# Kernel tuning notes

Measured on AMD Instinct MI355X. Metric: run time of the kernel, lower is better.

## Reference

```python
import jax, jax.numpy as jnp
import numpy as np

D_MODEL = 1024
NUM_HEADS = 16
HEAD_DIM = D_MODEL // NUM_HEADS


def setup_inputs() -> dict:
    key = jax.random.key(0)
    ks = jax.random.split(key, 9)
    B, S, D = 4, 2048, D_MODEL
    scale = 1.0 / np.sqrt(D)
    x = jax.random.normal(ks[0], (B, S, D), dtype=jnp.float32)
    wq = jax.random.normal(ks[1], (D, D), dtype=jnp.float32) * scale
    wk = jax.random.normal(ks[2], (D, D), dtype=jnp.float32) * scale
    wv = jax.random.normal(ks[3], (D, D), dtype=jnp.float32) * scale
    wo = jax.random.normal(ks[4], (D, D), dtype=jnp.float32) * scale
    bq = jax.random.normal(ks[5], (D,), dtype=jnp.float32) * 0.02
    bk = jax.random.normal(ks[6], (D,), dtype=jnp.float32) * 0.02
    bv = jax.random.normal(ks[7], (D,), dtype=jnp.float32) * 0.02
    bo = jax.random.normal(ks[8], (D,), dtype=jnp.float32) * 0.02
    return {"x": x, "wq": wq, "bq": bq, "wk": wk, "bk": bk,
            "wv": wv, "bv": bv, "wo": wo, "bo": bo}


def _split_heads(t):  # [B,S,D] -> [B,H,S,Dh]
    B, S, _ = t.shape
    return t.reshape(B, S, NUM_HEADS, HEAD_DIM).transpose(0, 2, 1, 3)


def reference(x, wq, bq, wk, bk, wv, bv, wo, bo):
    B, S, D = x.shape
    q = _split_heads(x @ wq + bq)  # [B,H,S,Dh]
    k = _split_heads(x @ wk + bk)
    v = _split_heads(x @ wv + bv)
    scores = jnp.einsum("bhqd,bhkd->bhqk", q, k) / jnp.sqrt(
        jnp.asarray(HEAD_DIM, dtype=x.dtype))
    causal = jnp.tril(jnp.ones((S, S), dtype=bool))  # [S,S]
    scores = jnp.where(causal, scores, jnp.finfo(scores.dtype).min)
    attn = jax.nn.softmax(scores, axis=-1)
    ctx = jnp.einsum("bhqk,bhkd->bhqd", attn, v)  # [B,H,S,Dh]
    ctx = ctx.transpose(0, 2, 1, 3).reshape(B, S, D)
    return ctx @ wo + bo
```

## Files before the change

kernel.cpp:

```cpp
#include <hip/hip_runtime.h>
#include <hip/hip_bf16.h>
#include <stdint.h>

#define DMODEL 1024
#define NH 16
#define DH 64
#define BATCH 4
#define SEQ 2048

#if __has_builtin(__builtin_amdgcn_exp2f)
#define EXP2F(x) __builtin_amdgcn_exp2f(x)
#else
#define EXP2F(x) exp2f(x)
#endif

typedef __attribute__((ext_vector_type(8))) short short8;
typedef __attribute__((ext_vector_type(4))) float f32x4;
typedef __attribute__((ext_vector_type(4))) ushort ushort4v;

__device__ __forceinline__ ushort f2bf(float f) {
    union { float f; unsigned u; } v; v.f = f;
    unsigned r = v.u + 0x7fffu + ((v.u >> 16) & 1u);
    return (ushort)(r >> 16);
}

__global__ __launch_bounds__(256) void prep_inputs(
    const float* __restrict__ x, ushort* __restrict__ xbf,
    const float* __restrict__ s0, const float* __restrict__ s1,
    const float* __restrict__ s2, const float* __restrict__ s3,
    ushort* __restrict__ d0, ushort* __restrict__ d1,
    ushort* __restrict__ d2, ushort* __restrict__ d3) {
    __shared__ ushort tile[64][65];
    const int bid = blockIdx.x;
    if (bid < 4096) {
        const size_t i = ((size_t)bid * 256 + threadIdx.x) * 8;
        float4 a = *(const float4*)(x + i);
        float4 b = *(const float4*)(x + i + 4);
        short8 r;
        r[0] = (short)f2bf(a.x); r[1] = (short)f2bf(a.y);
        r[2] = (short)f2bf(a.z); r[3] = (short)f2bf(a.w);
        r[4] = (short)f2bf(b.x); r[5] = (short)f2bf(b.y);
        r[6] = (short)f2bf(b.z); r[7] = (short)f2bf(b.w);
        *(short8*)(xbf + i) = r;
        return;
    }
    const int r = bid - 4096;
    const int z = r >> 8;
    const float* src = (z == 0) ? s0 : (z == 1) ? s1 : (z == 2) ? s2 : s3;
    ushort* dst = (z == 0) ? d0 : (z == 1) ? d1 : (z == 2) ? d2 : d3;
    const int bx = (r & 15) * 64;
    const int by = ((r >> 4) & 15) * 64;
    const int tx = threadIdx.x & 63, ty = threadIdx.x >> 6;
    #pragma unroll
    for (int i = 0; i < 64; i += 4)
        tile[ty + i][tx] = f2bf(src[(size_t)(by + ty + i) * DMODEL + bx + tx]);
    __syncthreads();
    #pragma unroll
    for (int i = 0; i < 64; i += 4)
        dst[(size_t)(bx + ty + i) * DMODEL + by + tx] = tile[tx][ty + i];
}

#define BK 32
#define NT 32

template <int MODE>
__global__ __launch_bounds__(256, 3) void gemm_tile(
    const ushort* __restrict__ A, const ushort* __restrict__ Bt,
    const float* __restrict__ b0, const float* __restrict__ b1,
    const float* __restrict__ b2,
    void* __restrict__ o0v, void* __restrict__ o1v, void* __restrict__ o2v) {
    __shared__ __align__(16) ushort lds[24576];
    const int tid  = threadIdx.x;
    const int lane = tid & 63;
    const int wv   = tid >> 6;

    const int bid = blockIdx.x;
    const int by  = ((bid & 7) << 3) | ((bid >> 3) & 7);
    const int bx  = bid >> 6;
    const int mBase = by * 128, nBase = bx * 128;

    const int wm = (wv >> 1) * 64;
    const int wn = (wv & 1) * 64;
    const int frow = lane & 15;
    const int fq   = lane >> 4;
    const int cA   = ((((fq ^ (frow >> 1)) & 3) << 1) | (frow & 1)) << 3;
    const int roff = (frow >> 1) * 64 + cA;

    const int sr   = tid >> 3;
    const int c8   = tid & 7;
    const int grow = (sr << 1) | (c8 & 1);
    const int gkc8 = (((c8 >> 1) ^ sr) & 3) * 8;
    const ushort* gA = A  + (size_t)(mBase + grow) * DMODEL + gkc8;
    const ushort* gB = Bt + (size_t)(nBase + grow) * DMODEL + gkc8;
    const int ldsw = wv * 512;

    f32x4 acc[4][4];
    #pragma unroll
    for (int i = 0; i < 4; ++i)
        #pragma unroll
        for (int j = 0; j < 4; ++j) acc[i][j] = (f32x4){0.f, 0.f, 0.f, 0.f};

#define STG(gp, off) __builtin_amdgcn_global_load_lds( \
    (const __attribute__((address_space(1))) void*)(gp), \
    (__attribute__((address_space(3))) void*)&lds[(off) + ldsw], 16, 0, 0)
#define STAGE_A(sb, u, h) STG(gA + (size_t)(h) * 64 * DMODEL + (u) * BK, \
                              (sb) + (h) * 2048)
#define STAGE_B(sb, u, h) STG(gB + (size_t)(h) * 64 * DMODEL + (u) * BK, \
                              (sb) + 4096 + (h) * 2048)

    STAGE_A(0, 0, 0); STAGE_A(0, 0, 1); STAGE_B(0, 0, 0); STAGE_B(0, 0, 1);
    STAGE_A(8192, 1, 0); STAGE_A(8192, 1, 1);
    STAGE_B(8192, 1, 0); STAGE_B(8192, 1, 1);
    asm volatile("s_waitcnt vmcnt(4)" ::: "memory");
    __builtin_amdgcn_s_barrier();

    int sc = 0;
    #pragma unroll 1
    for (int u = 0; u < NT; ++u) {
        const int scB = sc * 8192;
        const int sp  = (sc == 0) ? 2 : sc - 1;
        const int spB = sp * 8192;
        const ushort* bufA = &lds[scB + wm * 32];
        const ushort* bufB = &lds[scB + 4096 + wn * 32];

        if (u + 2 < NT) {
            STAGE_A(spB, u + 2, 0); STAGE_A(spB, u + 2, 1);
            STAGE_B(spB, u + 2, 0); STAGE_B(spB, u + 2, 1);
        }

        short8 af[4], bf[4];
        #pragma unroll
        for (int f = 0; f < 4; ++f)
            af[f] = *(const short8*)&bufA[f * 512 + roff];
        #pragma unroll
        for (int j = 0; j < 4; ++j)
            bf[j] = *(const short8*)&bufB[j * 512 + roff];
        __builtin_amdgcn_s_setprio(1);
        #pragma unroll
        for (int f = 0; f < 4; ++f)
            #pragma unroll
            for (int j = 0; j < 4; ++j)
                acc[f][j] = __builtin_amdgcn_mfma_f32_16x16x32_bf16(
                    af[f], bf[j], acc[f][j], 0, 0, 0);
        __builtin_amdgcn_s_setprio(0);

        if (u + 2 < NT)       { asm volatile("s_waitcnt vmcnt(4)" ::: "memory"); }
        else if (u + 2 == NT) { asm volatile("s_waitcnt vmcnt(0)" ::: "memory"); }
        __builtin_amdgcn_s_barrier();
        sc = (sc == 2) ? 0 : sc + 1;
    }
#undef STG
#undef STAGE_A
#undef STAGE_B

    const int orow = fq * 4;
    const int ocol = frow;

    if (MODE == 1) {
        #pragma unroll
        for (int i = 0; i < 4; ++i)
            #pragma unroll
            for (int j = 0; j < 4; ++j)
                #pragma unroll
                for (int r = 0; r < 4; ++r) {
                    const int m = mBase + wm + i * 16 + orow + r;
                    const int n = nBase + wn + j * 16 + ocol;
                    ((float*)o0v)[(size_t)m * DMODEL + n] = acc[i][j][r] + b0[n];
                }
        return;
    }

    __syncthreads();
    ushort* o0 = (ushort*)o0v; ushort* o1 = (ushort*)o1v; ushort* o2 = (ushort*)o2v;
    ushort* sw = &lds[wv * 1152];
    const int mat = nBase >> 10;
    const int nb0 = (nBase & 1023) + wn;
    const int hb  = nb0 >> 6;
    const float* bp = (mat == 0) ? b0 : ((mat == 1) ? b1 : b2);
    float bj[4];
    #pragma unroll
    for (int j = 0; j < 4; ++j) bj[j] = bp[nb0 + j * 16 + ocol];
    const int mrow = mBase + wm;
    const int bbq = mrow >> 11;
    const int s0w = mrow & 2047;
    const float qscale = (mat == 0) ? 0.1803368801f : 1.0f;

    if (mat < 2) {
        ushort* obase = ((mat == 0) ? o0 : o1) +
                        ((size_t)(bbq * NH + hb) * SEQ + s0w) * DH;
        const int row = lane >> 2, cc = lane & 3;
        #pragma unroll
        for (int i = 0; i < 4; ++i) {
            #pragma unroll
            for (int j = 0; j < 4; ++j)
                #pragma unroll
                for (int r = 0; r < 4; ++r)
                    sw[(orow + r) * 72 + j * 16 + ocol] =
                        f2bf((acc[i][j][r] + bj[j]) * qscale);
            asm volatile("s_waitcnt lgkmcnt(0)" ::: "memory");
            #pragma unroll
            for (int p = 0; p < 2; ++p) {
                short8 v8 = *(const short8*)&sw[row * 72 + cc * 8 + p * 32];
                *(short8*)&obase[(size_t)(i * 16 + row) * DH + cc * 8 + p * 32] = v8;
            }
            asm volatile("s_waitcnt lgkmcnt(0)" ::: "memory");
        }
    } else {
        const int rowd = lane >> 2, scl = lane & 3;
        #pragma unroll
        for (int j = 0; j < 4; ++j) {
            #pragma unroll
            for (int ii = 0; ii < 4; ++ii)
                #pragma unroll
                for (int r = 0; r < 4; ++r)
                    sw[ocol * 72 + ii * 16 + orow + r] = f2bf(acc[ii][j][r] + bj[j]);
            asm volatile("s_waitcnt lgkmcnt(0)" ::: "memory");
            ushort* vbase = o2 + ((size_t)(bbq * NH + hb) * DH + j * 16 + rowd) * SEQ + s0w;
            #pragma unroll
            for (int p = 0; p < 2; ++p) {
                short8 v8 = *(const short8*)&sw[rowd * 72 + scl * 8 + p * 32];
                *(short8*)&vbase[scl * 8 + p * 32] = v8;
            }
            asm volatile("s_waitcnt lgkmcnt(0)" ::: "memory");
        }
    }
}

#define PSTR 72
__global__ __launch_bounds__(512, 6) void flash_attn(
    const ushort* __restrict__ Q, const ushort* __restrict__ K,
    const ushort* __restrict__ Vt, ushort* __restrict__ ctx) {
    __shared__ __align__(16) ushort Ks[2][4096];
    __shared__ __align__(16) ushort Vs[2][4096];
    __shared__ __align__(16) ushort plds[8][16 * PSTR];
    const int tid  = threadIdx.x;
    const int lane = tid & 63;
    const int wv   = tid >> 6;
    const int bh   = blockIdx.x & 63;
    const int Jp   = blockIdx.x >> 6;
    const int bb = bh >> 4, h = bh & 15;

    const ushort* Qb = Q + (size_t)bh * SEQ * DH;
    const ushort* Kb = K + (size_t)bh * SEQ * DH;
    const ushort* Vb = Vt + (size_t)bh * DH * SEQ;

    const int frow = lane & 15;
    const int fq   = lane >> 4;
    const int trow = tid >> 3;
    const int tcho = ((tid & 7) ^ (trow & 7)) * 8;
    const int ldsw = wv * 512;

    short8 ones;
    #pragma unroll
    for (int i = 0; i < 8; ++i) ones[i] = (short)0x3F80;

#define FA_STG(gp, lp) __builtin_amdgcn_global_load_lds( \
    (const __attribute__((address_space(1))) void*)(gp), \
    (__attribute__((address_space(3))) void*)(lp), 16, 0, 0)

    #pragma unroll 1
    for (int half = 0; half < 2; ++half) {
        const int J = half ? (15 - Jp) : Jp;
        const int ktmax = 2 * J + 1;
        const int q0 = J * 128 + (wv >> 2) * 64 + (wv & 3) * 16;
        const int qmax = q0 + 15;

        short8 qf[2];
        #pragma unroll
        for (int ks = 0; ks < 2; ++ks)
            qf[ks] = *(const short8*)&Qb[(size_t)(q0 + frow) * DH + ks * 32 + fq * 8];

        f32x4 o[4], lacc;
        #pragma unroll
        for (int t = 0; t < 4; ++t) o[t] = (f32x4){0.f, 0.f, 0.f, 0.f};
        lacc = (f32x4){0.f, 0.f, 0.f, 0.f};

        FA_STG(Kb + (size_t)trow * DH + tcho, &Ks[0][ldsw]);
        FA_STG(Vb + (size_t)trow * SEQ + tcho, &Vs[0][ldsw]);
        asm volatile("s_waitcnt vmcnt(0)" ::: "memory");
        __builtin_amdgcn_s_barrier();

        #pragma unroll 1
        for (int kt = 0; kt <= ktmax; ++kt) {
            const int k0 = kt * 64;
            const int cur = kt & 1;
            if (kt < ktmax) {
                const int kn = k0 + 64;
                FA_STG(Kb + (size_t)(kn + trow) * DH + tcho, &Ks[cur ^ 1][ldsw]);
                FA_STG(Vb + (size_t)trow * SEQ + kn + tcho, &Vs[cur ^ 1][ldsw]);
            }
            const ushort* Ksc = Ks[cur];
            const ushort* Vsc = Vs[cur];

            if (k0 <= qmax) {
            if (k0 + 64 <= q0) {
                f32x4 sacc[4];
                #pragma unroll
                for (int nt = 0; nt < 4; ++nt) sacc[nt] = (f32x4){0.f, 0.f, 0.f, 0.f};
                #pragma unroll
                for (int nt = 0; nt < 4; ++nt) {
                    const int row = nt * 16 + frow, r7 = row & 7;
                    #pragma unroll
                    for (int ks = 0; ks < 2; ++ks) {
                        short8 kf = *(const short8*)
                            &Ksc[(row >> 3) * 512 + r7 * 64 + (((ks * 4 + fq) ^ r7) * 8)];
                        sacc[nt] = __builtin_amdgcn_mfma_f32_16x16x32_bf16(kf, qf[ks],
                                                                          sacc[nt], 0, 0, 0);
                    }
                }
                #pragma unroll
                for (int nt = 0; nt < 4; ++nt) {
                    float p0 = EXP2F(sacc[nt][0]);
                    float p1 = EXP2F(sacc[nt][1]);
                    float p2 = EXP2F(sacc[nt][2]);
                    float p3 = EXP2F(sacc[nt][3]);
                    uint2 dw;
                    dw.x = __builtin_amdgcn_perm(__float_as_uint(p1), __float_as_uint(p0),
                                                 0x07060302u);
                    dw.y = __builtin_amdgcn_perm(__float_as_uint(p3), __float_as_uint(p2),
                                                 0x07060302u);
                    *(uint2*)&plds[wv][frow * PSTR + nt * 16 + fq * 4] = dw;
                }
                asm volatile("s_waitcnt lgkmcnt(0)" ::: "memory");
                #pragma unroll
                for (int kc = 0; kc < 2; ++kc) {
                    short8 pf = *(const short8*)&plds[wv][frow * PSTR + kc * 32 + fq * 8];
                    lacc = __builtin_amdgcn_mfma_f32_16x16x32_bf16(ones, pf, lacc, 0, 0, 0);
                    __builtin_amdgcn_s_setprio(1);
                    #pragma unroll
                    for (int t = 0; t < 4; ++t) {
                        const int row = t * 16 + frow, r7 = row & 7;
                        short8 vf = *(const short8*)
                            &Vsc[(row >> 3) * 512 + r7 * 64 + (((kc * 4 + fq) ^ r7) * 8)];
                        o[t] = __builtin_amdgcn_mfma_f32_16x16x32_bf16(vf, pf, o[t], 0, 0, 0);
                    }
                    __builtin_amdgcn_s_setprio(0);
                }
            } else {
                const int qrow = q0 + frow;
                f32x4 sacc[4];
                #pragma unroll
                for (int nt = 0; nt < 4; ++nt) sacc[nt] = (f32x4){0.f, 0.f, 0.f, 0.f};
                #pragma unroll
                for (int nt = 0; nt < 4; ++nt)
                    if (k0 + nt * 16 <= qmax) {
                        const int row = nt * 16 + frow, r7 = row & 7;
                        #pragma unroll
                        for (int ks = 0; ks < 2; ++ks) {
                            short8 kf = *(const short8*)
                                &Ksc[(row >> 3) * 512 + r7 * 64 + (((ks * 4 + fq) ^ r7) * 8)];
                            sacc[nt] = __builtin_amdgcn_mfma_f32_16x16x32_bf16(kf, qf[ks],
                                                                              sacc[nt], 0, 0, 0);
                        }
                    }
                #pragma unroll
                for (int nt = 0; nt < 4; ++nt) {
                    uint2 dw; dw.x = 0u; dw.y = 0u;
                    if (k0 + nt * 16 <= qmax) {
                        float pp[4];
                        #pragma unroll
                        for (int r = 0; r < 4; ++r) {
                            const float e = EXP2F(sacc[nt][r]);
                            pp[r] = (k0 + nt * 16 + fq * 4 + r <= qrow) ? e : 0.f;
                        }
                        dw.x = __builtin_amdgcn_perm(__float_as_uint(pp[1]),
                                                     __float_as_uint(pp[0]), 0x07060302u);
                        dw.y = __builtin_amdgcn_perm(__float_as_uint(pp[3]),
                                                     __float_as_uint(pp[2]), 0x07060302u);
                    }
                    *(uint2*)&plds[wv][frow * PSTR + nt * 16 + fq * 4] = dw;
                }
                asm volatile("s_waitcnt lgkmcnt(0)" ::: "memory");
                #pragma unroll
                for (int kc = 0; kc < 2; ++kc) {
                    if (k0 + kc * 32 <= qmax) {
                        short8 pf = *(const short8*)&plds[wv][frow * PSTR + kc * 32 + fq * 8];
                        lacc = __builtin_amdgcn_mfma_f32_16x16x32_bf16(ones, pf, lacc, 0, 0, 0);
                        #pragma unroll
                        for (int t = 0; t < 4; ++t) {
                            const int row = t * 16 + frow, r7 = row & 7;
                            short8 vf = *(const short8*)
                                &Vsc[(row >> 3) * 512 + r7 * 64 + (((kc * 4 + fq) ^ r7) * 8)];
                            o[t] = __builtin_amdgcn_mfma_f32_16x16x32_bf16(vf, pf, o[t], 0, 0, 0);
                        }
                    }
                }
            }
            }

            asm volatile("s_waitcnt lgkmcnt(0) vmcnt(0)" ::: "memory");
            __builtin_amdgcn_s_barrier();
        }

        const float inv = 1.0f / lacc[0];
        const int qrow = q0 + frow;
        ushort* cp = ctx + (size_t)(bb * SEQ + qrow) * DMODEL + h * DH;
        #pragma unroll
        for (int t = 0; t < 4; ++t) {
            ushort4v ov;
            #pragma unroll
            for (int r = 0; r < 4; ++r) ov[r] = f2bf(o[t][r] * inv);
            *(ushort4v*)&cp[t * 16 + fq * 4] = ov;
        }
    }
#undef FA_STG
}

extern "C" void kernel_launch(void* const* d_in, const int* in_sizes, int n_in,
                              void* d_out, int out_size, void* d_ws, size_t ws_size,
                              hipStream_t stream) {
    const float* x  = (const float*)d_in[0];
    const float* wq = (const float*)d_in[1];
    const float* bq = (const float*)d_in[2];
    const float* wk = (const float*)d_in[3];
    const float* bk = (const float*)d_in[4];
    const float* wvp = (const float*)d_in[5];
    const float* bv = (const float*)d_in[6];
    const float* wo = (const float*)d_in[7];
    const float* bo = (const float*)d_in[8];
    float* out = (float*)d_out;
    ushort* ws = (ushort*)d_ws;

    const size_t QSZ = (size_t)BATCH * NH * SEQ * DH;
    ushort* xbf   = ws;
    ushort* qws   = ws + QSZ;
    ushort* kws   = ws + 2 * QSZ;
    ushort* vtws  = ws + 3 * QSZ;
    ushort* ctxws = ws + 4 * QSZ;
    ushort* wtqkv = ws + 5 * QSZ;
    ushort* wto   = wtqkv + 3 * (size_t)DMODEL * DMODEL;

    dim3 tb(256);
    prep_inputs<<<dim3(5120), tb, 0, stream>>>(
        x, xbf, wq, wk, wvp, wo,
        wtqkv, wtqkv + (size_t)DMODEL * DMODEL, wtqkv + 2 * (size_t)DMODEL * DMODEL, wto);

    gemm_tile<0><<<dim3(1536), tb, 0, stream>>>(xbf, wtqkv, bq, bk, bv,
                                                qws, kws, vtws);
    flash_attn<<<dim3(512), dim3(512), 0, stream>>>(qws, kws, vtws, ctxws);
    gemm_tile<1><<<dim3(512), tb, 0, stream>>>(ctxws, wto, bo, nullptr, nullptr,
                                               out, nullptr, nullptr);
}
```

Baseline: 241.2 us.

## Switch GEMM to BK=64 double-buffered pipeline with new LDS swizzle

Doubles the K-step per iteration to 64 and halves the number of loop iterations. The triple-buffered, distance-2 prefetch becomes a double-buffered, distance-1 prefetch with a full vmcnt(0) wait each step. The LDS layout and XOR swizzle are redone for 64-wide rows. The goal is fewer barriers and more MFMA work per sync. The cost is a larger LDS footprint (64KB), occupancy dropping from 3 to 2 blocks, and less latency hiding.

```diff
diff --git a/kernel.cpp b/kernel.cpp
--- a/kernel.cpp
+++ b/kernel.cpp
@@ -60,16 +60,16 @@
         dst[(size_t)(bx + ty + i) * DMODEL + by + tx] = tile[tx][ty + i];
 }
 
-#define BK 32
-#define NT 32
+#define BK 64
+#define NT 16
 
 template <int MODE>
-__global__ __launch_bounds__(256, 3) void gemm_tile(
+__global__ __launch_bounds__(256, 2) void gemm_tile(
     const ushort* __restrict__ A, const ushort* __restrict__ Bt,
     const float* __restrict__ b0, const float* __restrict__ b1,
     const float* __restrict__ b2,
     void* __restrict__ o0v, void* __restrict__ o1v, void* __restrict__ o2v) {
-    __shared__ __align__(16) ushort lds[24576];
+    __shared__ __align__(16) ushort lds[32768];
     const int tid  = threadIdx.x;
     const int lane = tid & 63;
     const int wv   = tid >> 6;
@@ -83,15 +83,14 @@
     const int wn = (wv & 1) * 64;
     const int frow = lane & 15;
     const int fq   = lane >> 4;
-    const int cA   = ((((fq ^ (frow >> 1)) & 3) << 1) | (frow & 1)) << 3;
-    const int roff = (frow >> 1) * 64 + cA;
-
-    const int sr   = tid >> 3;
-    const int c8   = tid & 7;
-    const int grow = (sr << 1) | (c8 & 1);
-    const int gkc8 = (((c8 >> 1) ^ sr) & 3) * 8;
-    const ushort* gA = A  + (size_t)(mBase + grow) * DMODEL + gkc8;
-    const ushort* gB = Bt + (size_t)(nBase + grow) * DMODEL + gkc8;
+    const int r7x  = frow & 7;
+    const int swk0 = (fq ^ r7x) << 3;
+    const int swk1 = ((4 + fq) ^ r7x) << 3;
+
+    const int trow = tid >> 3;
+    const int tcho = ((tid & 7) ^ (trow & 7)) * 8;
+    const ushort* gA = A  + (size_t)(mBase + trow) * DMODEL + tcho;
+    const ushort* gB = Bt + (size_t)(nBase + trow) * DMODEL + tcho;
     const int ldsw = wv * 512;
 
     f32x4 acc[4][4];
@@ -103,55 +102,58 @@
 #define STG(gp, off) __builtin_amdgcn_global_load_lds( \
     (const __attribute__((address_space(1))) void*)(gp), \
     (__attribute__((address_space(3))) void*)&lds[(off) + ldsw], 16, 0, 0)
-#define STAGE_A(sb, u, h) STG(gA + (size_t)(h) * 64 * DMODEL + (u) * BK, \
-                              (sb) + (h) * 2048)
-#define STAGE_B(sb, u, h) STG(gB + (size_t)(h) * 64 * DMODEL + (u) * BK, \
-                              (sb) + 4096 + (h) * 2048)
-
-    STAGE_A(0, 0, 0); STAGE_A(0, 0, 1); STAGE_B(0, 0, 0); STAGE_B(0, 0, 1);
-    STAGE_A(8192, 1, 0); STAGE_A(8192, 1, 1);
-    STAGE_B(8192, 1, 0); STAGE_B(8192, 1, 1);
-    asm volatile("s_waitcnt vmcnt(4)" ::: "memory");
+#define STAGE_A(sb, u, g) STG(gA + (size_t)(g) * 32 * DMODEL + (u) * BK, \
+                              (sb) + (g) * 2048)
+#define STAGE_B(sb, u, g) STG(gB + (size_t)(g) * 32 * DMODEL + (u) * BK, \
+                              (sb) + 8192 + (g) * 2048)
+#define STAGE_ALL(sb, u) { \
+    STAGE_A(sb, u, 0); STAGE_A(sb, u, 1); STAGE_A(sb, u, 2); STAGE_A(sb, u, 3); \
+    STAGE_B(sb, u, 0); STAGE_B(sb, u, 1); STAGE_B(sb, u, 2); STAGE_B(sb, u, 3); }
+
+    STAGE_ALL(0, 0);
+    asm volatile("s_waitcnt vmcnt(0)" ::: "memory");
     __builtin_amdgcn_s_barrier();
 
-    int sc = 0;
     #pragma unroll 1
     for (int u = 0; u < NT; ++u) {
-        const int scB = sc * 8192;
-        const int sp  = (sc == 0) ? 2 : sc - 1;
-        const int spB = sp * 8192;
-        const ushort* bufA = &lds[scB + wm * 32];
-        const ushort* bufB = &lds[scB + 4096 + wn * 32];
-
-        if (u + 2 < NT) {
-            STAGE_A(spB, u + 2, 0); STAGE_A(spB, u + 2, 1);
-            STAGE_B(spB, u + 2, 0); STAGE_B(spB, u + 2, 1);
-        }
-
-        short8 af[4], bf[4];
+        const int cb = (u & 1) * 16384;
+        const int nb = 16384 - cb;
+
+        if (u + 1 < NT) STAGE_ALL(nb, u + 1);
+
+        const ushort* bufA = &lds[cb + wm * 64];
+        const ushort* bufB = &lds[cb + 8192 + wn * 64];
+        short8 af[4][2], bf[4][2];
+        #pragma unroll
+        for (int f = 0; f < 4; ++f) {
+            const int ro = (f * 16 + frow) * 64;
+            af[f][0] = *(const short8*)&bufA[ro + swk0];
+            af[f][1] = *(const short8*)&bufA[ro + swk1];
+        }
+        #pragma unroll
+        for (int j = 0; j < 4; ++j) {
+            const int ro = (j * 16 + frow) * 64;
+            bf[j][0] = *(const short8*)&bufB[ro + swk0];
+            bf[j][1] = *(const short8*)&bufB[ro + swk1];
+        }
+        __builtin_amdgcn_s_setprio(1);
         #pragma unroll
         for (int f = 0; f < 4; ++f)
-            af[f] = *(const short8*)&bufA[f * 512 + roff];
-        #pragma unroll
-        for (int j = 0; j < 4; ++j)
-            bf[j] = *(const short8*)&bufB[j * 512 + roff];
-        __builtin_amdgcn_s_setprio(1);
-        #pragma unroll
-        for (int f = 0; f < 4; ++f)
             #pragma unroll
             for (int j = 0; j < 4; ++j)
-                acc[f][j] = __builtin_amdgcn_mfma_f32_16x16x32_bf16(
-                    af[f], bf[j], acc[f][j], 0, 0, 0);
+                #pragma unroll
+                for (int ks = 0; ks < 2; ++ks)
+                    acc[f][j] = __builtin_amdgcn_mfma_f32_16x16x32_bf16(
+                        af[f][ks], bf[j][ks], acc[f][j], 0, 0, 0);
         __builtin_amdgcn_s_setprio(0);
 
-        if (u + 2 < NT)       { asm volatile("s_waitcnt vmcnt(4)" ::: "memory"); }
-        else if (u + 2 == NT) { asm volatile("s_waitcnt vmcnt(0)" ::: "memory"); }
+        asm volatile("s_waitcnt vmcnt(0)" ::: "memory");
         __builtin_amdgcn_s_barrier();
-        sc = (sc == 2) ? 0 : sc + 1;
     }
 #undef STG
 #undef STAGE_A
 #undef STAGE_B
+#undef STAGE_ALL
 
     const int orow = fq * 4;
     const int ocol = frow;
```

Measured after the change: 232.3 us. -3.7%, faster.
